# Performance work log

Measured on AMD Instinct MI355X. Metric: run time of the kernel, lower is better.

Reference implementation:

```python
import jax, jax.numpy as jnp
import numpy as np
from jax import lax

D_IN = 512     # input_dim
H_DIM = 1024   # hidden_dim
N_BATCH = 1024
T_STEPS = 64


def setup_inputs() -> dict:
    key = jax.random.key(0)
    ks = jax.random.split(key, 6)
    x = jax.random.normal(ks[0], (N_BATCH, T_STEPS, D_IN), dtype=jnp.float32)
    A = jax.random.normal(ks[1], (N_BATCH, H_DIM, 4, 4), dtype=jnp.float32)
    # parameters, init as in torch module
    Wx = jax.random.normal(ks[2], (D_IN, 4 * H_DIM), dtype=jnp.float32) / np.sqrt(D_IN)
    Wh = jax.random.normal(ks[3], (H_DIM, 4 * H_DIM), dtype=jnp.float32) / np.sqrt(H_DIM)
    Wattn = jax.random.normal(ks[4], (H_DIM, 4 * H_DIM), dtype=jnp.float32) / np.sqrt(H_DIM)
    b = jnp.zeros((4 * H_DIM,), dtype=jnp.float32)
    return {"x": x, "A": A, "Wx": Wx, "Wh": Wh, "Wattn": Wattn, "b": b}


def reference(x, A, Wx, Wh, Wattn, b):
    N, T, D = x.shape
    H = A.shape[1]
    Af = A.reshape(N, H, 16)              # (N, H, 16) flattened 4x4 grid
    h0 = Af.mean(axis=-1)                 # mean over spatial grid == mean(dim=(2,3))
    scale = 1.0 / jnp.sqrt(jnp.asarray(H, dtype=x.dtype))

    def step(carry, xt):
        h, c = carry
        # scaled dot-product attention over the 16 grid cells
        scores = jnp.einsum('nh,nhl->nl', h, Af) * scale   # (N, 16)
        w = jax.nn.softmax(scores, axis=-1)
        attn = jnp.einsum('nhl,nl->nh', Af, w)             # (N, H)
        a = xt @ Wx + h @ Wh + attn @ Wattn + b            # (N, 4H)
        ai, af, ao, ag = jnp.split(a, 4, axis=-1)
        i = jax.nn.sigmoid(ai)
        f = jax.nn.sigmoid(af)
        o = jax.nn.sigmoid(ao)
        g = jnp.tanh(ag)
        c_next = f * c + i * g
        h_next = o * jnp.tanh(c_next)
        return (h_next, c_next), h_next

    _, hs = lax.scan(step, (h0, h0), jnp.swapaxes(x, 0, 1))  # hs: (T, N, H)
    return jnp.swapaxes(hs, 0, 1)                            # (N, T, H)
```

## Files before the change

kernel.cpp:

```cpp
#include <hip/hip_runtime.h>
#include <cstdint>

#define NB    1024
#define TT    64
#define DIN   512
#define HD    1024
#define FH    4096
#define KTOT  2560

typedef _Float16 half8 __attribute__((ext_vector_type(8)));
typedef float floatx4 __attribute__((ext_vector_type(4)));

#define OFF_WT    ((size_t)0)
#define OFF_X16   ((size_t)20971520)
#define OFF_A16   ((size_t)88080384)
#define OFF_H16   ((size_t)121634816)
#define OFF_AT16  ((size_t)123731968)
#define OFF_HF    ((size_t)125829120)
#define OFF_C     ((size_t)130023424)
#define OFF_ABUF  ((size_t)134217728)

__device__ __forceinline__ void async_copy16(const void* g, void* l) {
    __builtin_amdgcn_global_load_lds(
        (const __attribute__((address_space(1))) void*)(uintptr_t)g,
        (__attribute__((address_space(3))) void*)(uintptr_t)l,
        16, 0, 0);
}

__global__ void k_convert_w(const float* __restrict__ Wx, const float* __restrict__ Wh,
                            const float* __restrict__ Wattn, _Float16* __restrict__ Wt) {
    __shared__ float tile[32][33];
    const int k0 = blockIdx.x * 32;
    const int c0 = blockIdx.y * 32;
    const int tx = threadIdx.x & 31;
    const int ty = threadIdx.x >> 5;
    const float* src; int kb;
    if (k0 < 512)       { src = Wx;    kb = k0; }
    else if (k0 < 1536) { src = Wh;    kb = k0 - 512; }
    else                { src = Wattn; kb = k0 - 1536; }
    #pragma unroll
    for (int r = ty; r < 32; r += 8)
        tile[r][tx] = src[(size_t)(kb + r) * FH + c0 + tx];
    __syncthreads();
    #pragma unroll
    for (int r = ty; r < 32; r += 8)
        Wt[(size_t)(c0 + r) * KTOT + k0 + tx] = (_Float16)tile[tx][r];
}

__global__ void k_convert(const float* __restrict__ src, _Float16* __restrict__ dst) {
    const size_t i = ((size_t)blockIdx.x * 256 + threadIdx.x) * 8;
    float4 v0 = *(const float4*)(src + i);
    float4 v1 = *(const float4*)(src + i + 4);
    half8 h;
    h[0] = (_Float16)v0.x; h[1] = (_Float16)v0.y; h[2] = (_Float16)v0.z; h[3] = (_Float16)v0.w;
    h[4] = (_Float16)v1.x; h[5] = (_Float16)v1.y; h[6] = (_Float16)v1.z; h[7] = (_Float16)v1.w;
    *(half8*)(dst + i) = h;
}

__global__ void k_init(const float* __restrict__ A, float* __restrict__ hf,
                       _Float16* __restrict__ h16, float* __restrict__ c) {
    const int idx = blockIdx.x * 256 + threadIdx.x;
    const float* a = A + (size_t)idx * 16;
    float s = 0.f;
    #pragma unroll
    for (int l = 0; l < 16; l++) s += a[l];
    const float m = s * (1.0f / 16.0f);
    hf[idx] = m; h16[idx] = (_Float16)m; c[idx] = m;
}

__device__ __forceinline__ void attn_phase(const _Float16* __restrict__ A16, int n,
                                           const float* hs ,
                                           float red[4][16] ,
                                           _Float16* __restrict__ at16) {
    const int tid = threadIdx.x, lane = tid & 63, wid = tid >> 6;
    float s[16];
    #pragma unroll
    for (int l = 0; l < 16; l++) s[l] = 0.f;
    half8 a0[4], a1[4];
    #pragma unroll
    for (int kk = 0; kk < 4; kk++) {
        const int r = kk * 256 + tid;
        const _Float16* ap = A16 + ((size_t)n * HD + r) * 16;
        a0[kk] = *(const half8*)ap;
        a1[kk] = *(const half8*)(ap + 8);
        const float hv = hs[r];
        #pragma unroll
        for (int l = 0; l < 8; l++) {
            s[l]     += hv * (float)a0[kk][l];
            s[l + 8] += hv * (float)a1[kk][l];
        }
    }
    #pragma unroll
    for (int l = 0; l < 16; l++)
        #pragma unroll
        for (int off = 32; off > 0; off >>= 1) s[l] += __shfl_down(s[l], off, 64);
    if (lane == 0) {
        #pragma unroll
        for (int l = 0; l < 16; l++) red[wid][l] = s[l];
    }
    __syncthreads();
    float w[16]; float mx = -1e30f;
    #pragma unroll
    for (int l = 0; l < 16; l++) {
        w[l] = (red[0][l] + red[1][l] + red[2][l] + red[3][l]) * 0.03125f;
        mx = fmaxf(mx, w[l]);
    }
    float sum = 0.f;
    #pragma unroll
    for (int l = 0; l < 16; l++) { w[l] = __expf(w[l] - mx); sum += w[l]; }
    const float inv = 1.0f / sum;
    #pragma unroll
    for (int l = 0; l < 16; l++) w[l] *= inv;
    #pragma unroll
    for (int kk = 0; kk < 4; kk++) {
        const int r = kk * 256 + tid;
        float v = 0.f;
        #pragma unroll
        for (int l = 0; l < 8; l++) v += (float)a0[kk][l] * w[l] + (float)a1[kk][l] * w[l + 8];
        at16[(size_t)n * HD + r] = (_Float16)v;
    }
}

__global__ void k_attn_boot(const _Float16* __restrict__ A16, const float* __restrict__ hf,
                            _Float16* __restrict__ at16) {
    __shared__ float hs[HD];
    __shared__ float red[4][16];
    const int n = blockIdx.x, tid = threadIdx.x;
    #pragma unroll
    for (int kk = 0; kk < 4; kk++) {
        const int r = kk * 256 + tid;
        hs[r] = hf[(size_t)n * HD + r];
    }
    __syncthreads();
    attn_phase(A16, n, hs, red, at16);
}

__global__ void k_cellattn(const float* __restrict__ abuf, const float* __restrict__ b,
                           const _Float16* __restrict__ A16,
                           float* __restrict__ c, _Float16* __restrict__ h16,
                           _Float16* __restrict__ at16, float* __restrict__ out, int t) {
    __shared__ float hs[HD];
    __shared__ float red[4][16];
    const int n = blockIdx.x, tid = threadIdx.x;
    #pragma unroll
    for (int kk = 0; kk < 4; kk++) {
        const int j = kk * 256 + tid;
        const size_t base = (size_t)n * FH + j;
        const float ai = abuf[base]        + b[j];
        const float af = abuf[base + 1024] + b[j + 1024];
        const float ao = abuf[base + 2048] + b[j + 2048];
        const float ag = abuf[base + 3072] + b[j + 3072];
        const float ig = 1.0f / (1.0f + __expf(-ai));
        const float fg = 1.0f / (1.0f + __expf(-af));
        const float og = 1.0f / (1.0f + __expf(-ao));
        const float gg = tanhf(ag);
        const int idx = n * HD + j;
        const float cn = fg * c[idx] + ig * gg;
        c[idx] = cn;
        const float hn = og * tanhf(cn);
        hs[j] = hn;
        h16[idx] = (_Float16)hn;
        out[(size_t)n * (TT * HD) + (size_t)t * HD + j] = hn;
    }
    if (t == TT - 1) return;
    __syncthreads();
    attn_phase(A16, n, hs, red, at16);
}

__launch_bounds__(256)
__global__ void k_gemm(const _Float16* __restrict__ xh, const _Float16* __restrict__ h16,
                       const _Float16* __restrict__ at16, const _Float16* __restrict__ Wt,
                       float* __restrict__ abuf, int t) {
    __shared__ _Float16 As[2][2][128 * 32];
    __shared__ _Float16 Bs[2][2][64 * 32];
    const int tid  = threadIdx.x;
    const int lane = tid & 63;
    const int w    = tid >> 6;
    const int g    = w >> 1;
    const int wm   = w & 1;
    const int bid = blockIdx.x;
    const int xcd = bid & 7;
    const int jj  = bid >> 3;
    const int bm0 = (jj & 7) * 128;
    const int bn0 = (xcd * 8 + (jj >> 3)) * 64;
    const int srow = lane >> 2;
    const int scol = (lane & 3) * 8;

    auto stage = [&](int it2) {
        const int p  = it2 & 1;
        const int kb = it2 * 64;
        #pragma unroll
        for (int s = 0; s < 2; s++) {
            const int k0 = kb + s * 32;
            const _Float16* abase; int astride, klocal;
            if (k0 < DIN)           { abase = xh + (size_t)t * DIN; astride = TT * DIN; klocal = k0; }
            else if (k0 < DIN + HD) { abase = h16;  astride = HD; klocal = k0 - DIN; }
            else                    { abase = at16; astride = HD; klocal = k0 - DIN - HD; }
            #pragma unroll
            for (int q = 0; q < 2; q++) {
                const int row = w * 32 + q * 16;
                async_copy16(abase + (size_t)(bm0 + row + srow) * astride + klocal + scol,
                             &As[p][s][row * 32]);
            }
            async_copy16(Wt + (size_t)(bn0 + w * 16 + srow) * KTOT + k0 + scol,
                         &Bs[p][s][(w * 16) * 32]);
        }
    };

    floatx4 acc[4][4];
    #pragma unroll
    for (int i = 0; i < 4; i++)
        #pragma unroll
        for (int j = 0; j < 4; j++) acc[i][j] = (floatx4)0.0f;

    stage(0);
    const int kq = (lane >> 4) * 8;
    const int rr = lane & 15;
    for (int it = 0; it < KTOT / 64; it++) {
        const int p = it & 1;
        __syncthreads();
        if (it < KTOT / 64 - 1) stage(it + 1);
        half8 af[4], bf[4];
        #pragma unroll
        for (int i = 0; i < 4; i++)
            af[i] = *(const half8*)&As[p][g][(wm * 64 + i * 16 + rr) * 32 + kq];
        #pragma unroll
        for (int j = 0; j < 4; j++)
            bf[j] = *(const half8*)&Bs[p][g][(j * 16 + rr) * 32 + kq];
        #pragma unroll
        for (int i = 0; i < 4; i++)
            #pragma unroll
            for (int j = 0; j < 4; j++)
                acc[i][j] = __builtin_amdgcn_mfma_f32_16x16x32_f16(af[i], bf[j], acc[i][j], 0, 0, 0);
    }

    __syncthreads();
    float* red = (float*)As;
    if (g == 1) {
        #pragma unroll
        for (int i = 0; i < 4; i++)
            #pragma unroll
            for (int j = 0; j < 4; j++)
                *(floatx4*)&red[((((wm * 4 + i) * 4 + j) * 64) + lane) * 4] = acc[i][j];
    }
    __syncthreads();
    if (g == 0) {
        #pragma unroll
        for (int i = 0; i < 4; i++)
            #pragma unroll
            for (int j = 0; j < 4; j++)
                acc[i][j] += *(const floatx4*)&red[((((wm * 4 + i) * 4 + j) * 64) + lane) * 4];
        const int q4 = (lane >> 4) * 4;
        const int cn = lane & 15;
        #pragma unroll
        for (int i = 0; i < 4; i++)
            #pragma unroll
            for (int j = 0; j < 4; j++)
                #pragma unroll
                for (int r = 0; r < 4; r++) {
                    const int row = bm0 + wm * 64 + i * 16 + q4 + r;
                    const int col = bn0 + j * 16 + cn;
                    abuf[(size_t)row * FH + col] = acc[i][j][r];
                }
    }
}

extern "C" void kernel_launch(void* const* d_in, const int* in_sizes, int n_in,
                              void* d_out, int out_size, void* d_ws, size_t ws_size,
                              hipStream_t stream) {
    const float* x     = (const float*)d_in[0];
    const float* A     = (const float*)d_in[1];
    const float* Wx    = (const float*)d_in[2];
    const float* Wh    = (const float*)d_in[3];
    const float* Wattn = (const float*)d_in[4];
    const float* b     = (const float*)d_in[5];
    float* out = (float*)d_out;

    uint8_t* ws = (uint8_t*)d_ws;
    _Float16* Wt   = (_Float16*)(ws + OFF_WT);
    _Float16* x16  = (_Float16*)(ws + OFF_X16);
    _Float16* A16  = (_Float16*)(ws + OFF_A16);
    _Float16* h16  = (_Float16*)(ws + OFF_H16);
    _Float16* at16 = (_Float16*)(ws + OFF_AT16);
    float*    hf   = (float*)(ws + OFF_HF);
    float*    c    = (float*)(ws + OFF_C);
    float*    abuf = (float*)(ws + OFF_ABUF);

    k_convert_w<<<dim3(KTOT / 32, FH / 32), 256, 0, stream>>>(Wx, Wh, Wattn, Wt);
    k_convert<<<(NB * TT * DIN) / 2048, 256, 0, stream>>>(x, x16);
    k_convert<<<(NB * HD * 16) / 2048, 256, 0, stream>>>(A, A16);
    k_init<<<(NB * HD) / 256, 256, 0, stream>>>(A, hf, h16, c);
    k_attn_boot<<<NB, 256, 0, stream>>>(A16, hf, at16);

    for (int t = 0; t < TT; t++) {
        k_gemm<<<dim3(512), 256, 0, stream>>>(x16, h16, at16, Wt, abuf, t);
        k_cellattn<<<NB, 256, 0, stream>>>(abuf, b, A16, c, h16, at16, out, t);
    }
}
```

Measured before the change: 3.516 ms.

## Triple-buffer A tiles and prefetch two stages ahead with explicit vmcnt waits

Splits the LDS staging into separate A and B loaders. A (activations) becomes triple-buffered and is prefetched two K-iterations ahead, while B (weights) stays double-buffered one ahead. The per-iteration __syncthreads is replaced by explicit s_waitcnt lgkmcnt/vmcnt plus s_barrier, so only the tiles needed next must have landed. This aims to hide more global-load latency, but raises LDS use from 48KB to 64KB per block, which may reduce resident blocks per CU.

Result: no change. 3.456 ms (-1.7%).

```diff
diff --git a/kernel.cpp b/kernel.cpp
--- a/kernel.cpp
+++ b/kernel.cpp
@@ -171,7 +171,7 @@
 __global__ void k_gemm(const _Float16* __restrict__ xh, const _Float16* __restrict__ h16,
                        const _Float16* __restrict__ at16, const _Float16* __restrict__ Wt,
                        float* __restrict__ abuf, int t) {
-    __shared__ _Float16 As[2][2][128 * 32];
+    __shared__ _Float16 As[3][2][128 * 32];
     __shared__ _Float16 Bs[2][2][64 * 32];
     const int tid  = threadIdx.x;
     const int lane = tid & 63;
@@ -186,8 +186,8 @@
     const int srow = lane >> 2;
     const int scol = (lane & 3) * 8;
 
-    auto stage = [&](int it2) {
-        const int p  = it2 & 1;
+    auto stageA = [&](int it2) {
+        const int p  = it2 % 3;
         const int kb = it2 * 64;
         #pragma unroll
         for (int s = 0; s < 2; s++) {
@@ -202,6 +202,14 @@
                 async_copy16(abase + (size_t)(bm0 + row + srow) * astride + klocal + scol,
                              &As[p][s][row * 32]);
             }
+        }
+    };
+    auto stageB = [&](int it2) {
+        const int p  = it2 & 1;
+        const int kb = it2 * 64;
+        #pragma unroll
+        for (int s = 0; s < 2; s++) {
+            const int k0 = kb + s * 32;
             async_copy16(Wt + (size_t)(bn0 + w * 16 + srow) * KTOT + k0 + scol,
                          &Bs[p][s][(w * 16) * 32]);
         }
@@ -213,25 +221,37 @@
         #pragma unroll
         for (int j = 0; j < 4; j++) acc[i][j] = (floatx4)0.0f;
 
-    stage(0);
+    stageB(0);
+    stageA(0);
+    stageA(1);
+    asm volatile("s_waitcnt vmcnt(4)" ::: "memory");
+    __builtin_amdgcn_s_barrier();
+
     const int kq = (lane >> 4) * 8;
     const int rr = lane & 15;
-    for (int it = 0; it < KTOT / 64; it++) {
-        const int p = it & 1;
-        __syncthreads();
-        if (it < KTOT / 64 - 1) stage(it + 1);
+    const int NT = KTOT / 64;
+    for (int it = 0; it < NT; it++) {
+        const int pa = it % 3;
+        const int pb = it & 1;
+        if (it + 1 < NT) stageB(it + 1);
+        if (it + 2 < NT) stageA(it + 2);
         half8 af[4], bf[4];
         #pragma unroll
         for (int i = 0; i < 4; i++)
-            af[i] = *(const half8*)&As[p][g][(wm * 64 + i * 16 + rr) * 32 + kq];
+            af[i] = *(const half8*)&As[pa][g][(wm * 64 + i * 16 + rr) * 32 + kq];
         #pragma unroll
         for (int j = 0; j < 4; j++)
-            bf[j] = *(const half8*)&Bs[p][g][(j * 16 + rr) * 32 + kq];
+            bf[j] = *(const half8*)&Bs[pb][g][(j * 16 + rr) * 32 + kq];
         #pragma unroll
         for (int i = 0; i < 4; i++)
             #pragma unroll
             for (int j = 0; j < 4; j++)
                 acc[i][j] = __builtin_amdgcn_mfma_f32_16x16x32_f16(af[i], bf[j], acc[i][j], 0, 0, 0);
+        if (it == NT - 1) break;
+        asm volatile("s_waitcnt lgkmcnt(0)" ::: "memory");
+        if (it + 2 < NT) asm volatile("s_waitcnt vmcnt(4)" ::: "memory");
+        else             asm volatile("s_waitcnt vmcnt(0)" ::: "memory");
+        __builtin_amdgcn_s_barrier();
     }
 
     __syncthreads();
```

## Enlarge GEMM tile to 128x128 with 512 threads and hand-placed waits

Applied to the files above, without the earlier changes.

The per-step GEMM now uses 128x128 output tiles across 8 waves (two K-split groups of four waves in a 2x2 layout) and 256 blocks instead of 512. This halves the number of blocks and raises operand reuse per tile. The main-loop __syncthreads is replaced by explicit vmcnt/lgkmcnt waits plus a barrier placed after the MFMAs. The cell kernel also swaps tanhf for an exp-based fast tanh. Risks are lower occupancy and fewer blocks than CUs on a 256-CU-class device, plus slightly reduced tanh accuracy.

Measured after the change: 3.627 ms. 1.03x slower.

```diff
diff --git a/kernel.cpp b/kernel.cpp
--- a/kernel.cpp
+++ b/kernel.cpp
@@ -25,6 +25,10 @@
         (const __attribute__((address_space(1))) void*)(uintptr_t)g,
         (__attribute__((address_space(3))) void*)(uintptr_t)l,
         16, 0, 0);
+}
+
+__device__ __forceinline__ float fast_tanh(float x) {
+    return 1.0f - 2.0f / (__expf(2.0f * x) + 1.0f);
 }
 
 __global__ void k_convert_w(const float* __restrict__ Wx, const float* __restrict__ Wh,
@@ -153,11 +157,11 @@
         const float ig = 1.0f / (1.0f + __expf(-ai));
         const float fg = 1.0f / (1.0f + __expf(-af));
         const float og = 1.0f / (1.0f + __expf(-ao));
-        const float gg = tanhf(ag);
+        const float gg = fast_tanh(ag);
         const int idx = n * HD + j;
         const float cn = fg * c[idx] + ig * gg;
         c[idx] = cn;
-        const float hn = og * tanhf(cn);
+        const float hn = og * fast_tanh(cn);
         hs[j] = hn;
         h16[idx] = (_Float16)hn;
         out[(size_t)n * (TT * HD) + (size_t)t * HD + j] = hn;
@@ -167,22 +171,25 @@
     attn_phase(A16, n, hs, red, at16);
 }
 
-__launch_bounds__(256)
+#define NTILES (KTOT / 64)
+__launch_bounds__(512, 2)
 __global__ void k_gemm(const _Float16* __restrict__ xh, const _Float16* __restrict__ h16,
                        const _Float16* __restrict__ at16, const _Float16* __restrict__ Wt,
                        float* __restrict__ abuf, int t) {
-    __shared__ _Float16 As[2][2][128 * 32];
-    __shared__ _Float16 Bs[2][2][64 * 32];
+    __shared__ _Float16 smem[32768];
+    _Float16* As = smem;
+    _Float16* Bs = smem + 16384;
     const int tid  = threadIdx.x;
     const int lane = tid & 63;
     const int w    = tid >> 6;
-    const int g    = w >> 1;
-    const int wm   = w & 1;
+    const int g    = w >> 2;
+    const int q    = w & 3;
+    const int wm   = q >> 1, wn = q & 1;
     const int bid = blockIdx.x;
     const int xcd = bid & 7;
     const int jj  = bid >> 3;
     const int bm0 = (jj & 7) * 128;
-    const int bn0 = (xcd * 8 + (jj >> 3)) * 64;
+    const int bn0 = (xcd * 4 + (jj >> 3)) * 128;
     const int srow = lane >> 2;
     const int scol = (lane & 3) * 8;
 
@@ -196,14 +203,10 @@
             if (k0 < DIN)           { abase = xh + (size_t)t * DIN; astride = TT * DIN; klocal = k0; }
             else if (k0 < DIN + HD) { abase = h16;  astride = HD; klocal = k0 - DIN; }
             else                    { abase = at16; astride = HD; klocal = k0 - DIN - HD; }
-            #pragma unroll
-            for (int q = 0; q < 2; q++) {
-                const int row = w * 32 + q * 16;
-                async_copy16(abase + (size_t)(bm0 + row + srow) * astride + klocal + scol,
-                             &As[p][s][row * 32]);
-            }
+            async_copy16(abase + (size_t)(bm0 + w * 16 + srow) * astride + klocal + scol,
+                         &As[(p * 2 + s) * 4096 + (w * 16) * 32]);
             async_copy16(Wt + (size_t)(bn0 + w * 16 + srow) * KTOT + k0 + scol,
-                         &Bs[p][s][(w * 16) * 32]);
+                         &Bs[(p * 2 + s) * 4096 + (w * 16) * 32]);
         }
     };
 
@@ -214,34 +217,40 @@
         for (int j = 0; j < 4; j++) acc[i][j] = (floatx4)0.0f;
 
     stage(0);
+    asm volatile("s_waitcnt vmcnt(0)" ::: "memory");
+    __builtin_amdgcn_s_barrier();
+
     const int kq = (lane >> 4) * 8;
     const int rr = lane & 15;
-    for (int it = 0; it < KTOT / 64; it++) {
+    for (int it = 0; it < NTILES; it++) {
         const int p = it & 1;
-        __syncthreads();
-        if (it < KTOT / 64 - 1) stage(it + 1);
+        if (it + 1 < NTILES) stage(it + 1);
         half8 af[4], bf[4];
         #pragma unroll
         for (int i = 0; i < 4; i++)
-            af[i] = *(const half8*)&As[p][g][(wm * 64 + i * 16 + rr) * 32 + kq];
+            af[i] = *(const half8*)&As[(p * 2 + g) * 4096 + (wm * 64 + i * 16 + rr) * 32 + kq];
         #pragma unroll
         for (int j = 0; j < 4; j++)
-            bf[j] = *(const half8*)&Bs[p][g][(j * 16 + rr) * 32 + kq];
+            bf[j] = *(const half8*)&Bs[(p * 2 + g) * 4096 + (wn * 64 + j * 16 + rr) * 32 + kq];
         #pragma unroll
         for (int i = 0; i < 4; i++)
             #pragma unroll
             for (int j = 0; j < 4; j++)
                 acc[i][j] = __builtin_amdgcn_mfma_f32_16x16x32_f16(af[i], bf[j], acc[i][j], 0, 0, 0);
-    }
-
-    __syncthreads();
-    float* red = (float*)As;
+        if (it == NTILES - 1) break;
+        asm volatile("s_waitcnt lgkmcnt(0)" ::: "memory");
+        asm volatile("s_waitcnt vmcnt(0)" ::: "memory");
+        __builtin_amdgcn_s_barrier();
+    }
+
+    __syncthreads();
+    float* red = (float*)smem;
     if (g == 1) {
         #pragma unroll
         for (int i = 0; i < 4; i++)
             #pragma unroll
             for (int j = 0; j < 4; j++)
-                *(floatx4*)&red[((((wm * 4 + i) * 4 + j) * 64) + lane) * 4] = acc[i][j];
+                *(floatx4*)&red[(((q * 4 + i) * 4 + j) * 64 + lane) * 4] = acc[i][j];
     }
     __syncthreads();
     if (g == 0) {
@@ -249,7 +258,7 @@
         for (int i = 0; i < 4; i++)
             #pragma unroll
             for (int j = 0; j < 4; j++)
-                acc[i][j] += *(const floatx4*)&red[((((wm * 4 + i) * 4 + j) * 64) + lane) * 4];
+                acc[i][j] += *(const floatx4*)&red[(((q * 4 + i) * 4 + j) * 64 + lane) * 4];
         const int q4 = (lane >> 4) * 4;
         const int cn = lane & 15;
         #pragma unroll
@@ -259,7 +268,7 @@
                 #pragma unroll
                 for (int r = 0; r < 4; r++) {
                     const int row = bm0 + wm * 64 + i * 16 + q4 + r;
-                    const int col = bn0 + j * 16 + cn;
+                    const int col = bn0 + wn * 64 + j * 16 + cn;
                     abuf[(size_t)row * FH + col] = acc[i][j][r];
                 }
     }
@@ -293,7 +302,7 @@
     k_attn_boot<<<NB, 256, 0, stream>>>(A16, hf, at16);
 
     for (int t = 0; t < TT; t++) {
-        k_gemm<<<dim3(512), 256, 0, stream>>>(x16, h16, at16, Wt, abuf, t);
+        k_gemm<<<dim3(256), 512, 0, stream>>>(x16, h16, at16, Wt, abuf, t);
         k_cellattn<<<NB, 256, 0, stream>>>(abuf, b, A16, c, h16, at16, out, t);
     }
 }
```
